# Kernel tuning notes

Hardware: AMD Instinct MI355X
Metric: run time of the kernel (lower is better)

Reference implementation:

```python
import jax, jax.numpy as jnp
import numpy as np

N_NODES = 100000
N_EDGES = 1600000
F = 128


def setup_inputs() -> dict:
    key = jax.random.key(0)
    ks = jax.random.split(key, 8)
    edge_src = jax.random.randint(ks[0], (N_EDGES,), 0, N_NODES, dtype=jnp.int32)
    edge_dst = jax.random.randint(ks[1], (N_EDGES,), 0, N_NODES, dtype=jnp.int32)
    edge_vals = jax.random.uniform(ks[2], (N_EDGES,), dtype=jnp.float32)
    feats = jax.random.normal(ks[3], (N_NODES, F), dtype=jnp.float32)
    s = 1.0 / np.sqrt(F)
    W1 = jax.random.normal(ks[4], (F, F), dtype=jnp.float32) * s
    b1 = jax.random.normal(ks[5], (F,), dtype=jnp.float32) * s
    W2 = jax.random.normal(ks[6], (F, F), dtype=jnp.float32) * s
    b2 = jax.random.normal(ks[7], (F,), dtype=jnp.float32) * s
    return {"edge_src": edge_src, "edge_dst": edge_dst, "edge_vals": edge_vals,
            "feats": feats, "W1": W1, "b1": b1, "W2": W2, "b2": b2}


def reference(edge_src, edge_dst, edge_vals, feats, W1, b1, W2, b2):
    # LE = L @ feats  (SpMM over COO edges: dst <- sum val * feats[src])
    msgs = edge_vals[:, None] * jnp.take(feats, edge_src, axis=0)  # [E, F]
    LE = jax.ops.segment_sum(msgs, edge_dst, num_segments=feats.shape[0])  # [N, F]
    # sf_E = (L + I) @ feats = LE + feats  (SelfLoop is identity)
    sf_E = LE + feats
    left_part = sf_E @ W1.T + b1          # W1(sf_E)
    E = LE * feats                        # torch.mul(LE, feats)
    right_part = E @ W2.T + b2            # W2(E)
    return left_part + right_part
```

## Files before the change

kernel.cpp:

```cpp
#include <hip/hip_runtime.h>

#define N_NODES 100000
#define N_EDGES 1600000
#define F 128
#define M_PAD 100032
#define NCB 782
#define CAP 2432
#define EPB 4096
#define MS_BLOCKS 391
#define FB_BLOCKS 6250
#define W_BLOCKS 64
#define CC_BLOCKS 4

typedef __attribute__((ext_vector_type(8))) short short8;
typedef __attribute__((ext_vector_type(4))) float float4v;

__device__ __forceinline__ unsigned pack_bf16(float x, float y) {
    unsigned ux = __float_as_uint(x), uy = __float_as_uint(y);
    ux = (ux + 0x7fffu + ((ux >> 16) & 1u)) >> 16;
    uy = (uy + 0x7fffu + ((uy >> 16) & 1u)) >> 16;
    return ux | (uy << 16);
}

__global__ __launch_bounds__(256) void prep_kernel(
    const float4* __restrict__ feats4, uint4* __restrict__ featsb4,
    const float* __restrict__ W1, const float* __restrict__ W2,
    unsigned* __restrict__ Wbu, int* __restrict__ ccur)
{
    int b = blockIdx.x, t = threadIdx.x;
    if (b < FB_BLOCKS) {
        int i = b * 256 + t;
        float4 v0 = feats4[2 * i], v1 = feats4[2 * i + 1];
        featsb4[i] = make_uint4(pack_bf16(v0.x, v0.y), pack_bf16(v0.z, v0.w),
                                pack_bf16(v1.x, v1.y), pack_bf16(v1.z, v1.w));
    } else if (b < FB_BLOCKS + W_BLOCKS) {
        int i = (b - FB_BLOCKS) * 256 + t;
        int j = i >> 7, c = i & 127;
        const float* s = (c < 64) ? &W1[j * 128 + 2 * c] : &W2[j * 128 + 2 * (c - 64)];
        Wbu[i] = pack_bf16(s[0], s[1]);
    } else {
        int i = (b - FB_BLOCKS - W_BLOCKS) * 256 + t;
        if (i < NCB) ccur[i] = i * CAP;
    }
}

__global__ __launch_bounds__(256) void passA_kernel(
    const int* __restrict__ esrc, const int* __restrict__ edst,
    const float* __restrict__ evals, int* __restrict__ ccur,
    int2* __restrict__ srtA)
{
    __shared__ int2 sv[EPB];
    __shared__ unsigned short bkt[EPB];
    __shared__ int h[NCB], lo[NCB];

    const int t = threadIdx.x;
    const int base = blockIdx.x * EPB;
    const int cnt = min(EPB, N_EDGES - base);

    for (int i = t; i < NCB; i += 256) h[i] = 0;
    __syncthreads();

    int rsrc[16], rdst[16], rrank[16];
    float rval[16];
#pragma unroll
    for (int i = 0; i < 16; i++) {
        int e = base + i * 256 + t;
        if (e < N_EDGES) {
            rsrc[i] = esrc[e];
            rdst[i] = edst[e];
            rval[i] = evals[e];
            rrank[i] = atomicAdd(&h[rdst[i] >> 7], 1);
        } else rdst[i] = -1;
    }
    __syncthreads();

    if (t < 64) {
        int carry = 0;
        for (int b0 = 0; b0 < NCB; b0 += 64) {
            int i = b0 + t;
            int x = (i < NCB) ? h[i] : 0;
            int v = x;
#pragma unroll
            for (int d = 1; d < 64; d <<= 1) {
                int y = __shfl_up(v, d);
                if (t >= d) v += y;
            }
            if (i < NCB) lo[i] = v - x + carry;
            carry += __shfl(v, 63);
        }
    }
    __syncthreads();

#pragma unroll
    for (int i = 0; i < 16; i++) {
        if (rdst[i] >= 0) {
            int b = rdst[i] >> 7;
            int s = lo[b] + rrank[i];
            sv[s]  = make_int2(rsrc[i] | ((rdst[i] & 127) << 24),
                               __float_as_int(rval[i]));
            bkt[s] = (unsigned short)b;
        }
    }
    __syncthreads();

    for (int b = t; b < NCB; b += 256) {
        int c = h[b];
        if (c) {
            int g = atomicAdd(&ccur[b], c);
            lo[b] = g - lo[b];
        }
    }
    __syncthreads();

    for (int s = t; s < cnt; s += 256)
        srtA[lo[bkt[s]] + s] = sv[s];
}

__global__ __launch_bounds__(256) void fused_gather_kernel(
    const int* __restrict__ ccur, const int2* __restrict__ srtA,
    const uint2* __restrict__ fb2,
    uint2* __restrict__ Abig2)
{
    __shared__ int2 list[CAP];
    __shared__ int hist[128], cur[128];

    const int t = threadIdx.x;
    const int b = blockIdx.x;
    const int base = b * CAP;
    const int cnt = ccur[b] - base;

    if (t < 128) hist[t] = 0;
    __syncthreads();

    for (int i = t; i < cnt; i += 256)
        atomicAdd(&hist[(unsigned)srtA[base + i].x >> 24], 1);
    __syncthreads();

    if (t < 64) {
        int carry = 0;
#pragma unroll
        for (int c = 0; c < 2; c++) {
            int i = c * 64 + t;
            int x = hist[i], v = x;
#pragma unroll
            for (int d = 1; d < 64; d <<= 1) {
                int y = __shfl_up(v, d);
                if (t >= d) v += y;
            }
            cur[i] = v - x + carry;
            carry += __shfl(v, 63);
        }
    }
    __syncthreads();

    for (int i = t; i < cnt; i += 256) {
        int2 e = srtA[base + i];
        int d = (unsigned)e.x >> 24;
        int pos = atomicAdd(&cur[d], 1);
        list[pos] = make_int2(e.x & 0x00FFFFFF, e.y);
    }
    __syncthreads();

    const int w = t >> 6;
    const int lane = t & 63;
    const int hh = lane >> 5;
    const int l = lane & 31;

    for (int np = 0; np < 32; np += 2) {
        const int nl = w * 32 + np + hh;
        const int end = cur[nl];
        int i = end - hist[nl];

        float a0 = 0.f, a1 = 0.f, a2 = 0.f, a3 = 0.f;
        for (; i + 3 < end; i += 4) {
            int2 e0 = list[i], e1 = list[i + 1], e2 = list[i + 2], e3 = list[i + 3];
            uint2 p0 = fb2[(size_t)e0.x * 32 + l];
            uint2 p1 = fb2[(size_t)e1.x * 32 + l];
            uint2 p2 = fb2[(size_t)e2.x * 32 + l];
            uint2 p3 = fb2[(size_t)e3.x * 32 + l];
            float v0 = __int_as_float(e0.y), v1 = __int_as_float(e1.y);
            float v2 = __int_as_float(e2.y), v3 = __int_as_float(e3.y);
            a0 += v0 * __uint_as_float(p0.x << 16) + v1 * __uint_as_float(p1.x << 16)
                + v2 * __uint_as_float(p2.x << 16) + v3 * __uint_as_float(p3.x << 16);
            a1 += v0 * __uint_as_float(p0.x & 0xffff0000u) + v1 * __uint_as_float(p1.x & 0xffff0000u)
                + v2 * __uint_as_float(p2.x & 0xffff0000u) + v3 * __uint_as_float(p3.x & 0xffff0000u);
            a2 += v0 * __uint_as_float(p0.y << 16) + v1 * __uint_as_float(p1.y << 16)
                + v2 * __uint_as_float(p2.y << 16) + v3 * __uint_as_float(p3.y << 16);
            a3 += v0 * __uint_as_float(p0.y & 0xffff0000u) + v1 * __uint_as_float(p1.y & 0xffff0000u)
                + v2 * __uint_as_float(p2.y & 0xffff0000u) + v3 * __uint_as_float(p3.y & 0xffff0000u);
        }
        for (; i < end; i++) {
            int2 e0 = list[i];
            uint2 p0 = fb2[(size_t)e0.x * 32 + l];
            float v0 = __int_as_float(e0.y);
            a0 += v0 * __uint_as_float(p0.x << 16);
            a1 += v0 * __uint_as_float(p0.x & 0xffff0000u);
            a2 += v0 * __uint_as_float(p0.y << 16);
            a3 += v0 * __uint_as_float(p0.y & 0xffff0000u);
        }

        const int gn = b * 128 + nl;
        if (gn < N_NODES) {
            uint2 pf = fb2[(size_t)gn * 32 + l];
            float f0 = __uint_as_float(pf.x << 16);
            float f1 = __uint_as_float(pf.x & 0xffff0000u);
            float f2v = __uint_as_float(pf.y << 16);
            float f3 = __uint_as_float(pf.y & 0xffff0000u);

            uint2 S, P;
            S.x = pack_bf16(a0 + f0, a1 + f1);  S.y = pack_bf16(a2 + f2v, a3 + f3);
            P.x = pack_bf16(a0 * f0, a1 * f1);  P.y = pack_bf16(a2 * f2v, a3 * f3);
            Abig2[(size_t)gn * 64 + l]      = S;
            Abig2[(size_t)gn * 64 + 32 + l] = P;
        }
    }
}

__global__ __launch_bounds__(256) void gemm_kernel(
    const unsigned short* __restrict__ Abig, const unsigned short* __restrict__ Wb,
    const float* __restrict__ b1, const float* __restrict__ b2,
    float* __restrict__ out)
{
    const int t = threadIdx.x;
    const int w = t >> 6, lane = t & 63;
    const int col = lane & 15;
    const int quad = lane >> 4;
    const int ko = quad * 8;
    const int m0 = blockIdx.x * 64 + w * 16;

    float4v acc[8];
#pragma unroll
    for (int j = 0; j < 8; j++) acc[j] = (float4v)(0.f);

    const unsigned short* arow = Abig + (size_t)(m0 + col) * 256 + ko;
#pragma unroll
    for (int k0 = 0; k0 < 8; k0++) {
        short8 a = *(const short8*)(arow + k0 * 32);
#pragma unroll
        for (int j = 0; j < 8; j++) {
            short8 b = *(const short8*)&Wb[(size_t)(j * 16 + col) * 256 + k0 * 32 + ko];
            acc[j] = __builtin_amdgcn_mfma_f32_16x16x32_bf16(a, b, acc[j], 0, 0, 0);
        }
    }

#pragma unroll
    for (int j = 0; j < 8; j++) {
        int n0 = j * 16 + col;
        float bb = b1[n0] + b2[n0];
#pragma unroll
        for (int r = 0; r < 4; r++) {
            int m = m0 + quad * 4 + r;
            if (m < N_NODES)
                __builtin_nontemporal_store(acc[j][r] + bb, &out[(size_t)m * F + n0]);
        }
    }
}

extern "C" void kernel_launch(void* const* d_in, const int* in_sizes, int n_in,
                              void* d_out, int out_size, void* d_ws, size_t ws_size,
                              hipStream_t stream) {
    const int*   edge_src  = (const int*)d_in[0];
    const int*   edge_dst  = (const int*)d_in[1];
    const float* edge_vals = (const float*)d_in[2];
    const float* feats     = (const float*)d_in[3];
    const float* W1        = (const float*)d_in[4];
    const float* b1        = (const float*)d_in[5];
    const float* W2        = (const float*)d_in[6];
    const float* b2        = (const float*)d_in[7];
    float* out = (float*)d_out;

    char* ws = (char*)d_ws;
    unsigned*       featsb = (unsigned*)      (ws);
    int2*           srtA   = (int2*)          (ws + 25600000);
    int*            ccur   = (int*)           (ws + 40814592);
    unsigned*       Wbu    = (unsigned*)      (ws + 40818688);
    unsigned short* Abig   = (unsigned short*)(ws + 40884224);

    prep_kernel<<<FB_BLOCKS + W_BLOCKS + CC_BLOCKS, 256, 0, stream>>>(
        (const float4*)feats, (uint4*)featsb, W1, W2, Wbu, ccur);

    passA_kernel<<<MS_BLOCKS, 256, 0, stream>>>(
        edge_src, edge_dst, edge_vals, ccur, srtA);

    fused_gather_kernel<<<NCB, 256, 0, stream>>>(
        ccur, srtA, (const uint2*)featsb, (uint2*)Abig);

    gemm_kernel<<<M_PAD / 64, 256, 0, stream>>>(
        Abig, (const unsigned short*)Wbu, b1, b2, out);
}
```

Baseline: 277.2 us.

## Fuse gather and GEMM into one kernel with LDS-staged bf16 A tile

```diff
diff --git a/kernel.cpp b/kernel.cpp
--- a/kernel.cpp
+++ b/kernel.cpp
@@ -14,6 +14,8 @@
 
 typedef __attribute__((ext_vector_type(8))) short short8;
 typedef __attribute__((ext_vector_type(4))) float float4v;
+
+#define SWZ(c, r) ((c) ^ (((r) & 7) << 3))
 
 __device__ __forceinline__ unsigned pack_bf16(float x, float y) {
     unsigned ux = __float_as_uint(x), uy = __float_as_uint(y);
@@ -116,24 +118,34 @@
         srtA[lo[bkt[s]] + s] = sv[s];
 }
 
-__global__ __launch_bounds__(256) void fused_gather_kernel(
+union SmemT {
+    struct {
+        int2 list[CAP];
+        int hist[128];
+        int cur[128];
+    } s;
+    unsigned short Amat[128][256];
+};
+
+__global__ __launch_bounds__(256) void fused_kernel(
     const int* __restrict__ ccur, const int2* __restrict__ srtA,
     const uint2* __restrict__ fb2,
-    uint2* __restrict__ Abig2)
+    const unsigned short* __restrict__ Wb,
+    const float* __restrict__ b1, const float* __restrict__ b2,
+    float* __restrict__ out)
 {
-    __shared__ int2 list[CAP];
-    __shared__ int hist[128], cur[128];
+    __shared__ SmemT u;
 
     const int t = threadIdx.x;
     const int b = blockIdx.x;
     const int base = b * CAP;
     const int cnt = ccur[b] - base;
 
-    if (t < 128) hist[t] = 0;
+    if (t < 128) u.s.hist[t] = 0;
     __syncthreads();
 
     for (int i = t; i < cnt; i += 256)
-        atomicAdd(&hist[(unsigned)srtA[base + i].x >> 24], 1);
+        atomicAdd(&u.s.hist[(unsigned)srtA[base + i].x >> 24], 1);
     __syncthreads();
 
     if (t < 64) {
@@ -141,13 +153,13 @@
 #pragma unroll
         for (int c = 0; c < 2; c++) {
             int i = c * 64 + t;
-            int x = hist[i], v = x;
+            int x = u.s.hist[i], v = x;
 #pragma unroll
             for (int d = 1; d < 64; d <<= 1) {
                 int y = __shfl_up(v, d);
                 if (t >= d) v += y;
             }
-            cur[i] = v - x + carry;
+            u.s.cur[i] = v - x + carry;
             carry += __shfl(v, 63);
         }
     }
@@ -156,8 +168,8 @@
     for (int i = t; i < cnt; i += 256) {
         int2 e = srtA[base + i];
         int d = (unsigned)e.x >> 24;
-        int pos = atomicAdd(&cur[d], 1);
-        list[pos] = make_int2(e.x & 0x00FFFFFF, e.y);
+        int pos = atomicAdd(&u.s.cur[d], 1);
+        u.s.list[pos] = make_int2(e.x & 0x00FFFFFF, e.y);
     }
     __syncthreads();
 
@@ -166,14 +178,18 @@
     const int hh = lane >> 5;
     const int l = lane & 31;
 
-    for (int np = 0; np < 32; np += 2) {
-        const int nl = w * 32 + np + hh;
-        const int end = cur[nl];
-        int i = end - hist[nl];
+    unsigned Sx[16], Sy[16], Px[16], Py[16];
+
+#pragma unroll
+    for (int ii = 0; ii < 16; ii++) {
+        const int nl = w * 32 + ii * 2 + hh;
+        const int end = u.s.cur[nl];
+        int i = end - u.s.hist[nl];
 
         float a0 = 0.f, a1 = 0.f, a2 = 0.f, a3 = 0.f;
         for (; i + 3 < end; i += 4) {
-            int2 e0 = list[i], e1 = list[i + 1], e2 = list[i + 2], e3 = list[i + 3];
+            int2 e0 = u.s.list[i], e1 = u.s.list[i + 1];
+            int2 e2 = u.s.list[i + 2], e3 = u.s.list[i + 3];
             uint2 p0 = fb2[(size_t)e0.x * 32 + l];
             uint2 p1 = fb2[(size_t)e1.x * 32 + l];
             uint2 p2 = fb2[(size_t)e2.x * 32 + l];
@@ -190,7 +206,7 @@
                 + v2 * __uint_as_float(p2.y & 0xffff0000u) + v3 * __uint_as_float(p3.y & 0xffff0000u);
         }
         for (; i < end; i++) {
-            int2 e0 = list[i];
+            int2 e0 = u.s.list[i];
             uint2 p0 = fb2[(size_t)e0.x * 32 + l];
             float v0 = __int_as_float(e0.y);
             a0 += v0 * __uint_as_float(p0.x << 16);
@@ -200,58 +216,60 @@
         }
 
         const int gn = b * 128 + nl;
-        if (gn < N_NODES) {
-            uint2 pf = fb2[(size_t)gn * 32 + l];
-            float f0 = __uint_as_float(pf.x << 16);
-            float f1 = __uint_as_float(pf.x & 0xffff0000u);
-            float f2v = __uint_as_float(pf.y << 16);
-            float f3 = __uint_as_float(pf.y & 0xffff0000u);
-
-            uint2 S, P;
-            S.x = pack_bf16(a0 + f0, a1 + f1);  S.y = pack_bf16(a2 + f2v, a3 + f3);
-            P.x = pack_bf16(a0 * f0, a1 * f1);  P.y = pack_bf16(a2 * f2v, a3 * f3);
-            Abig2[(size_t)gn * 64 + l]      = S;
-            Abig2[(size_t)gn * 64 + 32 + l] = P;
-        }
-    }
-}
-
-__global__ __launch_bounds__(256) void gemm_kernel(
-    const unsigned short* __restrict__ Abig, const unsigned short* __restrict__ Wb,
-    const float* __restrict__ b1, const float* __restrict__ b2,
-    float* __restrict__ out)
-{
-    const int t = threadIdx.x;
-    const int w = t >> 6, lane = t & 63;
+        uint2 pf = make_uint2(0u, 0u);
+        if (gn < N_NODES) pf = fb2[(size_t)gn * 32 + l];
+        float f0 = __uint_as_float(pf.x << 16);
+        float f1 = __uint_as_float(pf.x & 0xffff0000u);
+        float f2v = __uint_as_float(pf.y << 16);
+        float f3 = __uint_as_float(pf.y & 0xffff0000u);
+
+        Sx[ii] = pack_bf16(a0 + f0, a1 + f1);  Sy[ii] = pack_bf16(a2 + f2v, a3 + f3);
+        Px[ii] = pack_bf16(a0 * f0, a1 * f1);  Py[ii] = pack_bf16(a2 * f2v, a3 * f3);
+    }
+    __syncthreads();
+
+#pragma unroll
+    for (int ii = 0; ii < 16; ii++) {
+        const int nl = w * 32 + ii * 2 + hh;
+        *(uint2*)&u.Amat[nl][SWZ(4 * l, nl)]       = make_uint2(Sx[ii], Sy[ii]);
+        *(uint2*)&u.Amat[nl][SWZ(128 + 4 * l, nl)] = make_uint2(Px[ii], Py[ii]);
+    }
+    __syncthreads();
+
     const int col = lane & 15;
     const int quad = lane >> 4;
     const int ko = quad * 8;
-    const int m0 = blockIdx.x * 64 + w * 16;
-
-    float4v acc[8];
-#pragma unroll
-    for (int j = 0; j < 8; j++) acc[j] = (float4v)(0.f);
-
-    const unsigned short* arow = Abig + (size_t)(m0 + col) * 256 + ko;
+    const int r0 = w * 32;
+
+    float4v acc0[8], acc1[8];
+#pragma unroll
+    for (int j = 0; j < 8; j++) { acc0[j] = (float4v)(0.f); acc1[j] = (float4v)(0.f); }
+
 #pragma unroll
     for (int k0 = 0; k0 < 8; k0++) {
-        short8 a = *(const short8*)(arow + k0 * 32);
+        const int rA = r0 + col, rB = r0 + 16 + col;
+        short8 aA = *(const short8*)&u.Amat[rA][SWZ(k0 * 32 + ko, rA)];
+        short8 aB = *(const short8*)&u.Amat[rB][SWZ(k0 * 32 + ko, rB)];
 #pragma unroll
         for (int j = 0; j < 8; j++) {
-            short8 b = *(const short8*)&Wb[(size_t)(j * 16 + col) * 256 + k0 * 32 + ko];
-            acc[j] = __builtin_amdgcn_mfma_f32_16x16x32_bf16(a, b, acc[j], 0, 0, 0);
-        }
-    }
-
+            short8 bw = *(const short8*)&Wb[(size_t)(j * 16 + col) * 256 + k0 * 32 + ko];
+            acc0[j] = __builtin_amdgcn_mfma_f32_16x16x32_bf16(aA, bw, acc0[j], 0, 0, 0);
+            acc1[j] = __builtin_amdgcn_mfma_f32_16x16x32_bf16(aB, bw, acc1[j], 0, 0, 0);
+        }
+    }
+
+    const int gm0 = b * 128 + r0;
 #pragma unroll
     for (int j = 0; j < 8; j++) {
         int n0 = j * 16 + col;
         float bb = b1[n0] + b2[n0];
 #pragma unroll
         for (int r = 0; r < 4; r++) {
-            int m = m0 + quad * 4 + r;
+            int m = gm0 + quad * 4 + r;
             if (m < N_NODES)
-                __builtin_nontemporal_store(acc[j][r] + bb, &out[(size_t)m * F + n0]);
+                __builtin_nontemporal_store(acc0[j][r] + bb, &out[(size_t)m * F + n0]);
+            if (m + 16 < N_NODES)
+                __builtin_nontemporal_store(acc1[j][r] + bb, &out[(size_t)(m + 16) * F + n0]);
         }
     }
 }
@@ -274,7 +292,6 @@
     int2*           srtA   = (int2*)          (ws + 25600000);
     int*            ccur   = (int*)           (ws + 40814592);
     unsigned*       Wbu    = (unsigned*)      (ws + 40818688);
-    unsigned short* Abig   = (unsigned short*)(ws + 40884224);
 
     prep_kernel<<<FB_BLOCKS + W_BLOCKS + CC_BLOCKS, 256, 0, stream>>>(
         (const float4*)feats, (uint4*)featsb, W1, W2, Wbu, ccur);
@@ -282,9 +299,6 @@
     passA_kernel<<<MS_BLOCKS, 256, 0, stream>>>(
         edge_src, edge_dst, edge_vals, ccur, srtA);
 
-    fused_gather_kernel<<<NCB, 256, 0, stream>>>(
-        ccur, srtA, (const uint2*)featsb, (uint2*)Abig);
-
-    gemm_kernel<<<M_PAD / 64, 256, 0, stream>>>(
-        Abig, (const unsigned short*)Wbu, b1, b2, out);
-}
+    fused_kernel<<<NCB, 256, 0, stream>>>(
+        ccur, srtA, (const uint2*)featsb, (const unsigned short*)Wbu, b1, b2, out);
+}
```

Result: no change. 280.9 us (+1.3%).

## Fold bf16 conversion into bucket pass and split gather blocks in half

Applied to the files above, without the earlier changes.

```diff
diff --git a/kernel.cpp b/kernel.cpp
--- a/kernel.cpp
+++ b/kernel.cpp
@@ -8,9 +8,8 @@
 #define CAP 2432
 #define EPB 4096
 #define MS_BLOCKS 391
-#define FB_BLOCKS 6250
-#define W_BLOCKS 64
-#define CC_BLOCKS 4
+#define FCHUNK 4093
+#define LCAP 1536
 
 typedef __attribute__((ext_vector_type(8))) short short8;
 typedef __attribute__((ext_vector_type(4))) float float4v;
@@ -22,39 +21,21 @@
     return ux | (uy << 16);
 }
 
-__global__ __launch_bounds__(256) void prep_kernel(
-    const float4* __restrict__ feats4, uint4* __restrict__ featsb4,
-    const float* __restrict__ W1, const float* __restrict__ W2,
-    unsigned* __restrict__ Wbu, int* __restrict__ ccur)
-{
-    int b = blockIdx.x, t = threadIdx.x;
-    if (b < FB_BLOCKS) {
-        int i = b * 256 + t;
-        float4 v0 = feats4[2 * i], v1 = feats4[2 * i + 1];
-        featsb4[i] = make_uint4(pack_bf16(v0.x, v0.y), pack_bf16(v0.z, v0.w),
-                                pack_bf16(v1.x, v1.y), pack_bf16(v1.z, v1.w));
-    } else if (b < FB_BLOCKS + W_BLOCKS) {
-        int i = (b - FB_BLOCKS) * 256 + t;
-        int j = i >> 7, c = i & 127;
-        const float* s = (c < 64) ? &W1[j * 128 + 2 * c] : &W2[j * 128 + 2 * (c - 64)];
-        Wbu[i] = pack_bf16(s[0], s[1]);
-    } else {
-        int i = (b - FB_BLOCKS - W_BLOCKS) * 256 + t;
-        if (i < NCB) ccur[i] = i * CAP;
-    }
-}
-
 __global__ __launch_bounds__(256) void passA_kernel(
     const int* __restrict__ esrc, const int* __restrict__ edst,
     const float* __restrict__ evals, int* __restrict__ ccur,
-    int2* __restrict__ srtA)
+    int2* __restrict__ srtA,
+    const float4* __restrict__ feats4, uint4* __restrict__ featsb4,
+    const float* __restrict__ W1, const float* __restrict__ W2,
+    unsigned* __restrict__ Wbu)
 {
     __shared__ int2 sv[EPB];
     __shared__ unsigned short bkt[EPB];
     __shared__ int h[NCB], lo[NCB];
 
     const int t = threadIdx.x;
-    const int base = blockIdx.x * EPB;
+    const int blk = blockIdx.x;
+    const int base = blk * EPB;
     const int cnt = min(EPB, N_EDGES - base);
 
     for (int i = t; i < NCB; i += 256) h[i] = 0;
@@ -88,6 +69,24 @@
             if (i < NCB) lo[i] = v - x + carry;
             carry += __shfl(v, 63);
         }
+    } else {
+        const int tc = t - 64;
+        if (blk < 64) {
+            for (int i = tc; i < 256; i += 192) {
+                int gi = blk * 256 + i;
+                int j = gi >> 7, c = gi & 127;
+                const float* s = (c < 64) ? &W1[j * 128 + 2 * c]
+                                          : &W2[j * 128 + 2 * (c - 64)];
+                Wbu[gi] = pack_bf16(s[0], s[1]);
+            }
+        }
+        const int f0 = blk * FCHUNK;
+        const int fend = min(f0 + FCHUNK, 1600000);
+        for (int i = f0 + tc; i < fend; i += 192) {
+            float4 v0 = feats4[2 * i], v1 = feats4[2 * i + 1];
+            featsb4[i] = make_uint4(pack_bf16(v0.x, v0.y), pack_bf16(v0.z, v0.w),
+                                    pack_bf16(v1.x, v1.y), pack_bf16(v1.z, v1.w));
+        }
     }
     __syncthreads();
 
@@ -106,7 +105,7 @@
     for (int b = t; b < NCB; b += 256) {
         int c = h[b];
         if (c) {
-            int g = atomicAdd(&ccur[b], c);
+            int g = b * CAP + atomicAdd(&ccur[b], c);
             lo[b] = g - lo[b];
         }
     }
@@ -121,43 +120,43 @@
     const uint2* __restrict__ fb2,
     uint2* __restrict__ Abig2)
 {
-    __shared__ int2 list[CAP];
-    __shared__ int hist[128], cur[128];
+    __shared__ int hist[64], cur[64];
+    __shared__ int2 list[LCAP];
 
     const int t = threadIdx.x;
-    const int b = blockIdx.x;
+    const int bb = blockIdx.x;
+    const int b = bb >> 1;
+    const int hf = bb & 1;
     const int base = b * CAP;
-    const int cnt = ccur[b] - base;
-
-    if (t < 128) hist[t] = 0;
-    __syncthreads();
-
-    for (int i = t; i < cnt; i += 256)
-        atomicAdd(&hist[(unsigned)srtA[base + i].x >> 24], 1);
+    const int cnt = ccur[b];
+
+    if (t < 64) hist[t] = 0;
+    __syncthreads();
+
+    for (int i = t; i < cnt; i += 256) {
+        int d = (unsigned)srtA[base + i].x >> 24;
+        if ((d >> 6) == hf) atomicAdd(&hist[d & 63], 1);
+    }
     __syncthreads();
 
     if (t < 64) {
-        int carry = 0;
-#pragma unroll
-        for (int c = 0; c < 2; c++) {
-            int i = c * 64 + t;
-            int x = hist[i], v = x;
-#pragma unroll
-            for (int d = 1; d < 64; d <<= 1) {
-                int y = __shfl_up(v, d);
-                if (t >= d) v += y;
-            }
-            cur[i] = v - x + carry;
-            carry += __shfl(v, 63);
-        }
+        int x = hist[t], v = x;
+#pragma unroll
+        for (int d = 1; d < 64; d <<= 1) {
+            int y = __shfl_up(v, d);
+            if (t >= d) v += y;
+        }
+        cur[t] = v - x;
     }
     __syncthreads();
 
     for (int i = t; i < cnt; i += 256) {
         int2 e = srtA[base + i];
         int d = (unsigned)e.x >> 24;
-        int pos = atomicAdd(&cur[d], 1);
-        list[pos] = make_int2(e.x & 0x00FFFFFF, e.y);
+        if ((d >> 6) == hf) {
+            int pos = atomicAdd(&cur[d & 63], 1);
+            list[pos] = make_int2(e.x & 0x00FFFFFF, e.y);
+        }
     }
     __syncthreads();
 
@@ -166,8 +165,9 @@
     const int hh = lane >> 5;
     const int l = lane & 31;
 
-    for (int np = 0; np < 32; np += 2) {
-        const int nl = w * 32 + np + hh;
+#pragma unroll
+    for (int np = 0; np < 16; np += 2) {
+        const int nl = w * 16 + np + hh;
         const int end = cur[nl];
         int i = end - hist[nl];
 
@@ -199,7 +199,7 @@
             a3 += v0 * __uint_as_float(p0.y & 0xffff0000u);
         }
 
-        const int gn = b * 128 + nl;
+        const int gn = b * 128 + hf * 64 + nl;
         if (gn < N_NODES) {
             uint2 pf = fb2[(size_t)gn * 32 + l];
             float f0 = __uint_as_float(pf.x << 16);
@@ -276,13 +276,13 @@
     unsigned*       Wbu    = (unsigned*)      (ws + 40818688);
     unsigned short* Abig   = (unsigned short*)(ws + 40884224);
 
-    prep_kernel<<<FB_BLOCKS + W_BLOCKS + CC_BLOCKS, 256, 0, stream>>>(
-        (const float4*)feats, (uint4*)featsb, W1, W2, Wbu, ccur);
+    hipMemsetAsync(ccur, 0, NCB * sizeof(int), stream);
 
     passA_kernel<<<MS_BLOCKS, 256, 0, stream>>>(
-        edge_src, edge_dst, edge_vals, ccur, srtA);
-
-    fused_gather_kernel<<<NCB, 256, 0, stream>>>(
+        edge_src, edge_dst, edge_vals, ccur, srtA,
+        (const float4*)feats, (uint4*)featsb, W1, W2, Wbu);
+
+    fused_gather_kernel<<<2 * NCB, 256, 0, stream>>>(
         ccur, srtA, (const uint2*)featsb, (uint2*)Abig);
 
     gemm_kernel<<<M_PAD / 64, 256, 0, stream>>>(
```

Result: no change. 274.4 us (-1.0%).
